# Kernel tuning notes

Hardware: AMD Instinct MI355X
Metric: run time of the kernel (lower is better)

The kernel has to match this reference:

```python
import jax, jax.numpy as jnp
import numpy as np

FEAT_RES = 512
FEAT_DIM = 48
WIDTH = 128
IN_DIM = FEAT_DIM + 27 + 63  # 138
N_RAYS, N_SAMPLES = 4096, 128


def positional_encode(x, L):
    freqs = (2.0 ** jnp.arange(L)).astype(x.dtype)            # [L]
    xf = x[..., None, :] * freqs[:, None]                      # [..., L, 3]
    enc = jnp.concatenate([jnp.sin(xf), jnp.cos(xf)], axis=-1) # [..., L, 6]
    return jnp.concatenate([x, enc.reshape(x.shape[:-1] + (L * 6,))], axis=-1)


def grid_sample_bilinear(plane, gx, gy):
    # plane: [C, H, W]; gx, gy: [N, S] in [-1, 1]; align_corners=True, zeros padding
    H, W = plane.shape[-2], plane.shape[-1]
    ix = (gx + 1.0) * 0.5 * (W - 1)
    iy = (gy + 1.0) * 0.5 * (H - 1)
    x0 = jnp.floor(ix); y0 = jnp.floor(iy)
    x1 = x0 + 1.0;      y1 = y0 + 1.0
    wx1 = ix - x0; wx0 = 1.0 - wx1
    wy1 = iy - y0; wy0 = 1.0 - wy1

    def gather(xi, yi, w):
        valid = (xi >= 0) & (xi <= W - 1) & (yi >= 0) & (yi <= H - 1)
        xc = jnp.clip(xi, 0, W - 1).astype(jnp.int32)
        yc = jnp.clip(yi, 0, H - 1).astype(jnp.int32)
        v = plane[:, yc, xc]                                   # [C, N, S]
        return v * (w * valid.astype(w.dtype))[None]

    return (gather(x0, y0, wx0 * wy0) + gather(x1, y0, wx1 * wy0)
            + gather(x0, y1, wx0 * wy1) + gather(x1, y1, wx1 * wy1))


def setup_inputs() -> dict:
    key = jax.random.key(0)
    ks = jax.random.split(key, 12)
    x = jax.random.uniform(ks[0], (N_RAYS, N_SAMPLES, 3), jnp.float32, -3.0, 3.0)
    d = jax.random.normal(ks[1], (N_RAYS, 3), jnp.float32)
    d = d / jnp.linalg.norm(d, axis=-1, keepdims=True)
    feat = jax.random.normal(ks[2], (3, FEAT_DIM, FEAT_RES, FEAT_RES), jnp.float32)
    s = 0.05
    W0 = jax.random.normal(ks[3], (IN_DIM, WIDTH), jnp.float32) * s
    b0 = jnp.zeros((WIDTH,), jnp.float32)
    W1 = jax.random.normal(ks[4], (WIDTH, WIDTH), jnp.float32) * s
    b1 = jnp.zeros((WIDTH,), jnp.float32)
    W2 = jax.random.normal(ks[5], (WIDTH, WIDTH), jnp.float32) * s
    b2 = jnp.zeros((WIDTH,), jnp.float32)
    W3 = jax.random.normal(ks[6], (WIDTH, 4), jnp.float32) * s
    b3 = jnp.zeros((4,), jnp.float32)
    return {"x": x, "d": d, "feat": feat, "W0": W0, "b0": b0,
            "W1": W1, "b1": b1, "W2": W2, "b2": b2, "W3": W3, "b3": b3}


def reference(x, d, feat, W0, b0, W1, b1, W2, b2, W3, b3):
    x = x / 3.0                                                # [N, S, 3]
    f_xy = grid_sample_bilinear(feat[0], x[..., 0], x[..., 1])  # [C, N, S]
    f_yz = grid_sample_bilinear(feat[1], x[..., 1], x[..., 2])
    f_xz = grid_sample_bilinear(feat[2], x[..., 0], x[..., 2])
    f_sum = jnp.moveaxis(f_xy + f_yz + f_xz, 0, -1)            # [N, S, C]

    d_rep = jnp.broadcast_to(d[:, None, :], x.shape)           # [N, S, 3]
    h = jnp.concatenate([f_sum, positional_encode(d_rep, 4), positional_encode(x, 10)], axis=-1)

    h = jax.nn.relu(h @ W0 + b0)
    h = jax.nn.relu(h @ W1 + b1)
    h = jax.nn.relu(h @ W2 + b2)
    out = h @ W3 + b3                                          # [N, S, 4]
    return jnp.concatenate([out[..., :3], jax.nn.relu(out[..., 3:])], axis=-1)
```

## Files before the change

kernel.cpp:

```cpp
#include <hip/hip_runtime.h>
#include <hip/hip_bf16.h>
#include <hip/hip_fp16.h>
#include <cstdint>
#include <cstddef>

#define NPLANE 262144
#define HSTR 144
#define PW_LAYER 18432
#define NCELL 32768
#define NSAMP 524288
#define NRAY 4096

#define WS_FEAT_OFF 131072
#define FEAT_BYTES  75497472
#define WS_CNT_OFF  (WS_FEAT_OFF + FEAT_BYTES)
#define WS_OFFS_OFF (WS_CNT_OFF + 131072)
#define WS_XS_OFF   (WS_OFFS_OFF + 131072)
#define WS_PED_OFF  (WS_XS_OFF + (size_t)NSAMP*16)
#define WS_END      (WS_PED_OFF + (size_t)NRAY*28*2)

#define TRS_BLKS 3072
#define PREP_BLKS 216
#define PED_BLKS 16
#define K2_BLKS (1 + TRS_BLKS + PREP_BLKS + PED_BLKS)

typedef unsigned int uint;
typedef __attribute__((ext_vector_type(16))) float f32x16;
typedef _Float16 half8 __attribute__((ext_vector_type(8)));

__device__ __forceinline__ unsigned short f16u(float f){
    __half h = __float2half(f);
    return *reinterpret_cast<unsigned short*>(&h);
}
__device__ __forceinline__ f32x16 mfma16_(half8 a, half8 b, f32x16 c){
    return __builtin_amdgcn_mfma_f32_32x32x16_f16(a, b, c, 0,0,0);
}

__device__ __forceinline__ uint part3(uint v){
    v &= 0x3ff;
    v = (v | (v<<16)) & 0x030000FFu;
    v = (v | (v<<8))  & 0x0300F00Fu;
    v = (v | (v<<4))  & 0x030C30C3u;
    v = (v | (v<<2))  & 0x09249249u;
    return v;
}
__device__ __forceinline__ uint cellkey(float x0, float x1, float x2){
    const float s = 1.0f/3.0f;
    const int cx = min(max((int)((x0*s+1.0f)*16.0f),0),31);
    const int cy = min(max((int)((x1*s+1.0f)*16.0f),0),31);
    const int cz = min(max((int)((x2*s+1.0f)*16.0f),0),31);
    return part3((uint)cx) | (part3((uint)cy)<<1) | (part3((uint)cz)<<2);
}

__global__ __launch_bounds__(256) void hist_k(const float* __restrict__ x, uint* __restrict__ counts){
    const int i = blockIdx.x*256 + threadIdx.x;
    if (i >= NSAMP) return;
    atomicAdd(&counts[cellkey(x[3*i], x[3*i+1], x[3*i+2])], 1u);
}

__global__ __launch_bounds__(256) void prepass_k(const float* __restrict__ feat,
                                                 const float* __restrict__ W0,
                                                 const float* __restrict__ W1,
                                                 const float* __restrict__ W2,
                                                 const float* __restrict__ b0,
                                                 const float* __restrict__ b1,
                                                 const float* __restrict__ b2,
                                                 const float* __restrict__ d,
                                                 const uint* __restrict__ counts,
                                                 uint* __restrict__ offs,
                                                 unsigned short* __restrict__ featT,
                                                 unsigned short* __restrict__ wp,
                                                 unsigned short* __restrict__ ped){
    const int bid = blockIdx.x, tid = threadIdx.x;
    if (bid == 0){
        __shared__ uint ps[256];
        uint s = 0;
        for (int i=0;i<128;++i) s += counts[tid*128+i];
        ps[tid] = s; __syncthreads();
        for (int off=1; off<256; off<<=1){
            uint v = (tid>=off) ? ps[tid-off] : 0u;
            __syncthreads();
            ps[tid] += v;
            __syncthreads();
        }
        uint base = ps[tid] - s;
        for (int i=0;i<128;++i){ uint c = counts[tid*128+i]; offs[tid*128+i] = base; base += c; }
        return;
    }
    if (bid <= TRS_BLKS){
        __shared__ unsigned short lb[256*50];
        const int pos = (bid-1)*256 + tid;
        const int p  = pos >> 18;
        const int yx = pos & (NPLANE-1);
        const float* src = feat + (size_t)p*48*NPLANE + yx;
        #pragma unroll 4
        for (int c = 0; c < 48; ++c){
            lb[tid*50 + c] = f16u(src[(size_t)c*NPLANE]);
        }
        __syncthreads();
        uint4* dst = (uint4*)(featT + (size_t)(bid-1)*(256*48));
        #pragma unroll
        for (int m = 0; m < 6; ++m){
            const int u4 = tid + m*256;
            const int byteoff = u4*16;
            const int smp = byteoff/96;
            const int off = (byteoff%96) >> 2;
            const uint* rw = (const uint*)(lb + smp*50);
            uint4 val; val.x = rw[off]; val.y = rw[off+1]; val.z = rw[off+2]; val.w = rw[off+3];
            dst[u4] = val;
        }
        return;
    }
    if (bid <= TRS_BLKS + PREP_BLKS){
        const int idx = (bid - 1 - TRS_BLKS)*256 + tid;
        if (idx >= 3*PW_LAYER) return;
        const int L = idx / PW_LAYER, base = idx % PW_LAYER;
        const float* W = (L==0)? W0 : (L==1)? W1 : W2;
        const float* B = (L==0)? b0 : (L==1)? b1 : b2;
        const int KREAL = (L==0)? 138 : 128;
        const int e  = base & 7;
        const int l  = (base >> 3) & 63;
        const int fr = base >> 9;
        const int ks = fr >> 2, nt = fr & 3;
        const int k  = ks*16 + (l >> 5)*8 + e;
        const int n  = nt*32 + (l & 31);
        float v = 0.f;
        if (k < KREAL) v = W[k*128 + n];
        else if (k == KREAL) v = B[n];
        wp[idx] = f16u(v);
        return;
    }
    {
        const int ray = (bid - 1 - TRS_BLKS - PREP_BLKS)*256 + tid;
        if (ray >= NRAY) return;
        const float dv0 = d[ray*3], dv1 = d[ray*3+1], dv2 = d[ray*3+2];
        unsigned short* row = ped + ray*28;
        row[0]=f16u(dv0); row[1]=f16u(dv1); row[2]=f16u(dv2);
        #pragma unroll
        for (int l=0;l<4;++l){
            const float sc = (float)(1<<l);
            float sv, cv;
            __sincosf(dv0*sc, &sv, &cv); row[3+l*6+0]=f16u(sv); row[3+l*6+3]=f16u(cv);
            __sincosf(dv1*sc, &sv, &cv); row[3+l*6+1]=f16u(sv); row[3+l*6+4]=f16u(cv);
            __sincosf(dv2*sc, &sv, &cv); row[3+l*6+2]=f16u(sv); row[3+l*6+5]=f16u(cv);
        }
        row[27] = 0;
    }
}

__global__ __launch_bounds__(256) void scatter_k(const float* __restrict__ x, uint* __restrict__ offs,
                                                 float4* __restrict__ xs){
    const int i = blockIdx.x*256 + threadIdx.x;
    if (i >= NSAMP) return;
    const float x0 = x[3*i], x1 = x[3*i+1], x2 = x[3*i+2];
    const uint pos = atomicAdd(&offs[cellkey(x0,x1,x2)], 1u);
    xs[pos] = make_float4(x0, x1, x2, __int_as_float(i));
}

__device__ __forceinline__ void run_layer(unsigned short* Hw, const unsigned short* __restrict__ Wp,
                                          int lane, int ln31, int kg, const int* pr){
    const unsigned short* Hrow = Hw + ln31*HSTR;
    f32x16 acc[4];
    #pragma unroll
    for (int i=0;i<4;++i) acc[i] = (f32x16)0.f;
    #pragma unroll
    for (int h=0; h<2; ++h){
        half8 bf[10];
        #pragma unroll
        for (int i=0;i<10;++i){
            const int ks = i>>1, nt = 2*h + (i&1);
            bf[i] = *reinterpret_cast<const half8*>(Wp + (((ks*4+nt)*64 + lane) << 3));
        }
        #pragma unroll
        for (int ks=0; ks<5; ++ks){
            const half8 a = *reinterpret_cast<const half8*>(Hrow + ks*16 + kg*8);
            acc[2*h]   = mfma16_(a, bf[2*ks],   acc[2*h]);
            acc[2*h+1] = mfma16_(a, bf[2*ks+1], acc[2*h+1]);
        }
        #pragma unroll
        for (int i=0;i<8;++i){
            const int ks = 5 + (i>>1), nt = 2*h + (i&1);
            bf[i] = *reinterpret_cast<const half8*>(Wp + (((ks*4+nt)*64 + lane) << 3));
        }
        #pragma unroll
        for (int ks=5; ks<9; ++ks){
            const half8 a = *reinterpret_cast<const half8*>(Hrow + ks*16 + kg*8);
            acc[2*h]   = mfma16_(a, bf[2*(ks-5)],   acc[2*h]);
            acc[2*h+1] = mfma16_(a, bf[2*(ks-5)+1], acc[2*h+1]);
        }
    }
    #pragma unroll
    for (int nt=0;nt<4;++nt){
        #pragma unroll
        for (int r=0;r<16;++r){
            const int row = pr[r] >> 8;
            const int col = nt*32 + (pr[r] & 255);
            Hw[row*HSTR + col] = f16u(fmaxf(acc[nt][r], 0.f));
        }
    }
}

__global__ __launch_bounds__(128, 4) void nerf_mfma(
    const unsigned short* __restrict__ featT,
    const unsigned short* __restrict__ wp0, const unsigned short* __restrict__ wp1,
    const unsigned short* __restrict__ wp2,
    const float* __restrict__ W3, const float* __restrict__ b3,
    const float4* __restrict__ xs, const unsigned short* __restrict__ ped,
    float* __restrict__ out)
{
    __shared__ unsigned short H[64*HSTR];
    __shared__ uint sW3u[256];
    __shared__ float4 sX[64];

    const int tid  = threadIdx.x;
    const int wid  = tid >> 6, lane = tid & 63;
    const int ln31 = lane & 31, kg = lane >> 5;
    const int sbase = wid * 32;
    const int base = (((int)blockIdx.x & 7)*1024 + ((int)blockIdx.x >> 3))*64 + sbase;
    unsigned short* Hw = H + sbase*HSTR;

    half8 pa = (half8)0, pb = (half8)0, qa = (half8)0, qb = (half8)0;
    if (kg == 0){
        pa[0] = (_Float16)(float)ln31;
        pb[0] = (_Float16)1.0f;
        qa[0] = (_Float16)1.0f;
        qb[0] = (_Float16)(float)ln31;
    }
    const f32x16 zz = (f32x16)0.f;
    const f32x16 D1 = mfma16_(pa, pb, zz);
    const f32x16 D2 = mfma16_(qa, qb, zz);
    int pr[16];
    #pragma unroll
    for (int r=0;r<16;++r) pr[r] = (((int)D1[r]) << 8) | (int)D2[r];

    if (lane < 32) sX[sbase + lane] = xs[base + lane];
    #pragma unroll
    for (int j=0;j<2;++j){
        const int idx = lane*2 + j;
        const int i2 = wid*128 + idx;
        const int k = i2 >> 1, c = i2 & 1;
        sW3u[i2] = ((uint)f16u(W3[k*4 + 2*c])) | (((uint)f16u(W3[k*4 + 2*c + 1])) << 16);
    }

    #pragma unroll
    for (int rr=0; rr<2; ++rr){
        if (rr == 1 && lane >= 32) break;
        const int s32 = rr ? lane : ln31;
        const int m   = rr ? 2 : kg;
        const float4 xr = sX[sbase + s32];
        const float xn = ((m==0)? xr.x : (m==1)? xr.y : xr.z) * (1.0f/3.0f);
        unsigned short* row = H + (sbase+s32)*HSTR;
        row[75+m] = f16u(xn);
        float sv, cv;
        __sincosf(xn, &sv, &cv);
        #pragma unroll
        for (int l=0;l<10;++l){
            row[78+l*6+m]   = f16u(sv);
            row[78+l*6+3+m] = f16u(cv);
            const float s2v = 2.0f*sv*cv;
            const float c2v = 1.0f - 2.0f*sv*sv;
            sv = s2v; cv = c2v;
        }
    }

    {
        const int s32 = lane >> 1, hf = lane & 1;
        const int sid = __float_as_int(sX[sbase + s32].w);
        const uint* src = (const uint*)(ped + (sid >> 7)*28) + hf*7;
        uint* dstu = (uint*)(H + (sbase+s32)*HSTR + 48) + hf*7;
        if (hf == 0){
            #pragma unroll
            for (int i=0;i<7;++i) dstu[i] = src[i];
        } else {
            #pragma unroll
            for (int i=0;i<6;++i) dstu[i] = src[i];
            H[(sbase+s32)*HSTR + 74] = ((const unsigned short*)src)[12];
        }
    }

    if (lane < 32){
        *(uint*)(H + (sbase+lane)*HSTR + 138)  = 0x00003C00u;
        *(uint2*)(H + (sbase+lane)*HSTR + 140) = make_uint2(0u, 0u);
    }

    #pragma unroll
    for (int rr=0; rr<3; ++rr){
        const int u = rr*64 + lane;
        const int s32 = u/6, ch = u - s32*6;
        const float4 xr = sX[sbase + s32];
        const float xn0 = xr.x*(1.0f/3.0f);
        const float xn1 = xr.y*(1.0f/3.0f);
        const float xn2 = xr.z*(1.0f/3.0f);
        const int c0 = ch*8;
        __half2 acc[4];
        #pragma unroll
        for (int q=0;q<4;++q) acc[q] = __float2half2_rn(0.f);
        #pragma unroll
        for (int p=0;p<3;++p){
            const float gx = (p==1)? xn1 : xn0;
            const float gy = (p==0)? xn1 : xn2;
            const float ix = ((gx+1.0f)*0.5f)*511.0f;
            const float iy = ((gy+1.0f)*0.5f)*511.0f;
            const float fx0 = floorf(ix), fy0 = floorf(iy);
            const float wx1 = ix - fx0, wy1 = iy - fy0;
            const float wx0 = 1.0f-wx1, wy0 = 1.0f-wy1;
            const int x0i = (int)fx0, y0i = (int)fy0;
            const int x0c = min(max(x0i,0),511),   x1c = min(max(x0i+1,0),511);
            const int y0c = min(max(y0i,0),511),   y1c = min(max(y0i+1,0),511);
            const uint r0 = (uint)(p*NPLANE + y0c*512);
            const uint r1 = (uint)(p*NPLANE + y1c*512);
            const uint  av[4] = {(r0+x0c)*48u, (r0+x1c)*48u, (r1+x0c)*48u, (r1+x1c)*48u};
            const float wv[4] = {wx0*wy0, wx1*wy0, wx0*wy1, wx1*wy1};
            #pragma unroll
            for (int cr=0;cr<4;++cr){
                const uint4 uv = *(const uint4*)(featT + av[cr] + c0);
                const __half2 w2 = __float2half2_rn(wv[cr]);
                union { uint4 v; __half2 h[4]; } t; t.v = uv;
                acc[0] = __hfma2(t.h[0], w2, acc[0]);
                acc[1] = __hfma2(t.h[1], w2, acc[1]);
                acc[2] = __hfma2(t.h[2], w2, acc[2]);
                acc[3] = __hfma2(t.h[3], w2, acc[3]);
            }
        }
        union { __half2 h[4]; uint4 v; } pk;
        #pragma unroll
        for (int q=0;q<4;++q) pk.h[q] = acc[q];
        *(uint4*)(H + (sbase+s32)*HSTR + c0) = pk.v;
    }

    run_layer(Hw, wp0, lane, ln31, kg, pr);
    if (lane < 32) *(uint4*)(Hw + lane*HSTR + 128) = make_uint4(0x00003C00u,0u,0u,0u);
    else           *(uint4*)(Hw + ln31*HSTR + 136) = make_uint4(0u,0u,0u,0u);
    run_layer(Hw, wp1, lane, ln31, kg, pr);
    run_layer(Hw, wp2, lane, ln31, kg, pr);

    {
        const int s32 = lane >> 1, cp = lane & 1;
        const unsigned short* hrow = Hw + s32*HSTR;
        const int sid = __float_as_int(sX[sbase + s32].w);
        const int jp = 2*cp;
        const float2 b3v = *(const float2*)(b3 + jp);
        float a0 = b3v.x, a1 = b3v.y;
        #pragma unroll
        for (int q=0;q<16;++q){
            union { uint4 v; __half2 h[4]; } u;
            u.v = *(const uint4*)(hrow + q*8);
            const int k = q*8;
            #pragma unroll
            for (int j2=0;j2<4;++j2){
                const float2 f = __half22float2(u.h[j2]);
                const int k2 = k + j2*2;
                union { uint u32; __half2 h; } w0c, w1c;
                w0c.u32 = sW3u[(k2+0)*2+cp];
                w1c.u32 = sW3u[(k2+1)*2+cp];
                const float2 w0f = __half22float2(w0c.h);
                const float2 w1f = __half22float2(w1c.h);
                a0 += f.x*w0f.x + f.y*w1f.x;
                a1 += f.x*w0f.y + f.y*w1f.y;
            }
        }
        if (cp == 1) a1 = fmaxf(a1, 0.f);
        float2 o; o.x = a0; o.y = a1;
        *(float2*)(out + (size_t)sid*4 + jp) = o;
    }
}

#define STR 148
#define SBLK 64
template<int K4, int KTAIL>
__device__ __forceinline__ void mlp_layer_fb(float (*Hs)[STR], const float* __restrict__ W,
                                             const float* __restrict__ B, int tid){
    const int tx = tid & 31, ty = tid >> 5;
    const int s0 = ty*8, j0 = tx*4;
    float acc[8][4];
    #pragma unroll
    for (int i=0;i<8;++i){ acc[i][0]=0.f; acc[i][1]=0.f; acc[i][2]=0.f; acc[i][3]=0.f; }
    for (int kk = 0; kk < K4; ++kk){
        const int k = kk*4;
        const float4 wa = *(const float4*)(W + (size_t)(k+0)*128 + j0);
        const float4 wb = *(const float4*)(W + (size_t)(k+1)*128 + j0);
        const float4 wc = *(const float4*)(W + (size_t)(k+2)*128 + j0);
        const float4 wd = *(const float4*)(W + (size_t)(k+3)*128 + j0);
        #pragma unroll
        for (int i=0;i<8;++i){
            const float4 h = *(const float4*)&Hs[s0+i][k];
            acc[i][0] += h.x*wa.x + h.y*wb.x + h.z*wc.x + h.w*wd.x;
            acc[i][1] += h.x*wa.y + h.y*wb.y + h.z*wc.y + h.w*wd.y;
            acc[i][2] += h.x*wa.z + h.y*wb.z + h.z*wc.z + h.w*wd.z;
            acc[i][3] += h.x*wa.w + h.y*wb.w + h.z*wc.w + h.w*wd.w;
        }
    }
    #pragma unroll
    for (int t=0;t<KTAIL;++t){
        const int k = K4*4+t;
        const float4 wa = *(const float4*)(W + (size_t)k*128 + j0);
        #pragma unroll
        for (int i=0;i<8;++i){
            const float h = Hs[s0+i][k];
            acc[i][0] += h*wa.x; acc[i][1] += h*wa.y; acc[i][2] += h*wa.z; acc[i][3] += h*wa.w;
        }
    }
    const float4 bb = *(const float4*)(B + j0);
    __syncthreads();
    #pragma unroll
    for (int i=0;i<8;++i){
        float4 o;
        o.x = fmaxf(acc[i][0]+bb.x, 0.f);
        o.y = fmaxf(acc[i][1]+bb.y, 0.f);
        o.z = fmaxf(acc[i][2]+bb.z, 0.f);
        o.w = fmaxf(acc[i][3]+bb.w, 0.f);
        *(float4*)&Hs[s0+i][j0] = o;
    }
    __syncthreads();
}

__global__ __launch_bounds__(256) void nerf_fused_fb(
    const float* __restrict__ x, const float* __restrict__ d,
    const float* __restrict__ feat,
    const float* __restrict__ W0, const float* __restrict__ b0,
    const float* __restrict__ W1, const float* __restrict__ b1,
    const float* __restrict__ W2, const float* __restrict__ b2,
    const float* __restrict__ W3, const float* __restrict__ b3,
    float* __restrict__ out)
{
    __shared__ float Hs[SBLK][STR];
    __shared__ uint4  sA[3][SBLK];
    __shared__ float4 sW[3][SBLK];

    const int tid = threadIdx.x;
    const int g0 = blockIdx.x * SBLK;

    if (tid < 192){
        const int s = tid & 63, p = tid >> 6;
        const int g = g0 + s;
        const float xn0 = x[3*g+0]/3.0f, xn1 = x[3*g+1]/3.0f, xn2 = x[3*g+2]/3.0f;
        const float gx = (p==1)? xn1 : xn0;
        const float gy = (p==0)? xn1 : xn2;
        const float ix = ((gx+1.0f)*0.5f)*511.0f;
        const float iy = ((gy+1.0f)*0.5f)*511.0f;
        const float fx0 = floorf(ix), fy0 = floorf(iy);
        const float wx1 = ix - fx0, wy1 = iy - fy0;
        const float wx0 = 1.0f-wx1, wy0 = 1.0f-wy1;
        const int x0i = (int)fx0, y0i = (int)fy0;
        const int x0c = min(max(x0i,0),511),   x1c = min(max(x0i+1,0),511);
        const int y0c = min(max(y0i,0),511),   y1c = min(max(y0i+1,0),511);
        const uint bp = (uint)p*48u*NPLANE;
        sA[p][s] = make_uint4(bp + y0c*512 + x0c, bp + y0c*512 + x1c,
                              bp + y1c*512 + x0c, bp + y1c*512 + x1c);
        sW[p][s] = make_float4(wx0*wy0, wx1*wy0, wx0*wy1, wx1*wy1);
    }
    if (tid < 64){
        const int s = tid, g = g0 + s;
        float xn[3];
        xn[0]=x[3*g+0]/3.0f; xn[1]=x[3*g+1]/3.0f; xn[2]=x[3*g+2]/3.0f;
        Hs[s][75]=xn[0]; Hs[s][76]=xn[1]; Hs[s][77]=xn[2];
        float f = 1.0f;
        for (int l=0;l<10;++l){
            #pragma unroll
            for (int m=0;m<3;++m){
                const float a = xn[m]*f;
                Hs[s][78+l*6+m]   = sinf(a);
                Hs[s][78+l*6+3+m] = cosf(a);
            }
            f *= 2.0f;
        }
    } else if (tid < 91){
        const int k = tid-64;
        const int ray = g0 >> 7;
        float v;
        if (k < 3) v = d[ray*3+k];
        else {
            const int l=(k-3)/6, r=(k-3)%6;
            const float a = d[ray*3 + (r%3)] * (float)(1<<l);
            v = (r<3)? sinf(a) : cosf(a);
        }
        for (int s2=0;s2<64;++s2) Hs[s2][48+k]=v;
    }
    __syncthreads();

    for (int it = tid; it < 384; it += 256){
        const int s = it & 63;
        const int c0 = (it >> 6)*8;
        float acc[8];
        #pragma unroll
        for (int q=0;q<8;++q) acc[q]=0.f;
        #pragma unroll
        for (int p=0;p<3;++p){
            const uint4  aa = sA[p][s];
            const float4 ww = sW[p][s];
            const uint  av[4] = {aa.x,aa.y,aa.z,aa.w};
            const float wv[4] = {ww.x,ww.y,ww.z,ww.w};
            #pragma unroll
            for (int cr=0;cr<4;++cr){
                const float w = wv[cr];
                const float* bsrc = feat + av[cr] + (size_t)c0*NPLANE;
                #pragma unroll
                for (int q=0;q<8;++q) acc[q] += w*bsrc[(size_t)q*NPLANE];
            }
        }
        *(float4*)&Hs[s][c0]   = make_float4(acc[0],acc[1],acc[2],acc[3]);
        *(float4*)&Hs[s][c0+4] = make_float4(acc[4],acc[5],acc[6],acc[7]);
    }
    __syncthreads();

    mlp_layer_fb<34,2>(Hs, W0, b0, tid);
    mlp_layer_fb<32,0>(Hs, W1, b1, tid);
    mlp_layer_fb<32,0>(Hs, W2, b2, tid);

    {
        const int s = tid>>2, j = tid&3;
        float acc = 0.f;
        for (int kk=0; kk<32; ++kk){
            const float4 h = *(const float4*)&Hs[s][kk*4];
            const int k = kk*4;
            acc += h.x*W3[(k+0)*4+j] + h.y*W3[(k+1)*4+j]
                 + h.z*W3[(k+2)*4+j] + h.w*W3[(k+3)*4+j];
        }
        acc += b3[j];
        if (j==3) acc = fmaxf(acc, 0.f);
        out[(size_t)blockIdx.x*256 + tid] = acc;
    }
}

extern "C" void kernel_launch(void* const* d_in, const int* in_sizes, int n_in,
                              void* d_out, int out_size, void* d_ws, size_t ws_size,
                              hipStream_t stream){
    (void)in_sizes; (void)n_in; (void)out_size;
    const float* x    = (const float*)d_in[0];
    const float* ddir = (const float*)d_in[1];
    const float* feat = (const float*)d_in[2];
    const float* W0 = (const float*)d_in[3];  const float* b0 = (const float*)d_in[4];
    const float* W1 = (const float*)d_in[5];  const float* b1 = (const float*)d_in[6];
    const float* W2 = (const float*)d_in[7];  const float* b2 = (const float*)d_in[8];
    const float* W3 = (const float*)d_in[9];  const float* b3 = (const float*)d_in[10];
    float* out = (float*)d_out;

    char* wsb = (char*)d_ws;

    if (ws_size >= WS_END){
        unsigned short* wsu   = (unsigned short*)wsb;
        unsigned short* featT = (unsigned short*)(wsb + WS_FEAT_OFF);
        uint*   counts = (uint*)(wsb + WS_CNT_OFF);
        uint*   offs   = (uint*)(wsb + WS_OFFS_OFF);
        float4* xsrec  = (float4*)(wsb + WS_XS_OFF);
        unsigned short* ped = (unsigned short*)(wsb + WS_PED_OFF);
        hipMemsetAsync(counts, 0, NCELL*sizeof(uint), stream);
        hist_k<<<2048, 256, 0, stream>>>(x, counts);
        prepass_k<<<K2_BLKS, 256, 0, stream>>>(feat, W0, W1, W2, b0, b1, b2, ddir,
                                               counts, offs, featT, wsu, ped);
        scatter_k<<<2048, 256, 0, stream>>>(x, offs, xsrec);
        nerf_mfma<<<8192, 128, 0, stream>>>(featT,
                                            wsu, wsu + PW_LAYER, wsu + 2*PW_LAYER,
                                            W3, b3, xsrec, ped, out);
    } else {
        nerf_fused_fb<<<8192, 256, 0, stream>>>(x, ddir, feat,
                                                W0,b0,W1,b1,W2,b2,W3,b3, out);
    }
}
```

Before: 272.0 us.

## Split prefix scan out, fold scatter into prepass, halve MFMA accumulator live set

Moves the cell-count prefix scan into its own single-block kernel so the scatter work can be merged into the prepass launch, running scatter blocks alongside the feature transpose and weight packing. In the MLP layers, each half of the output columns now gets its own accumulator pair, and the first half's results are packed into half2 registers before the second pass. This lowers peak accumulator register pressure and could raise occupancy. The per-block W3 staging into shared memory is removed and the final layer reads fp32 W3 directly from global memory, which adds global loads in the epilogue.

```diff
diff --git a/kernel.cpp b/kernel.cpp
--- a/kernel.cpp
+++ b/kernel.cpp
@@ -22,7 +22,8 @@
 #define TRS_BLKS 3072
 #define PREP_BLKS 216
 #define PED_BLKS 16
-#define K2_BLKS (1 + TRS_BLKS + PREP_BLKS + PED_BLKS)
+#define SCAT_BLKS 2048
+#define K2_BLKS (TRS_BLKS + PREP_BLKS + PED_BLKS + SCAT_BLKS)
 
 typedef unsigned int uint;
 typedef __attribute__((ext_vector_type(16))) float f32x16;
@@ -56,6 +57,22 @@
     const int i = blockIdx.x*256 + threadIdx.x;
     if (i >= NSAMP) return;
     atomicAdd(&counts[cellkey(x[3*i], x[3*i+1], x[3*i+2])], 1u);
+}
+
+__global__ __launch_bounds__(256) void scan_k(const uint* __restrict__ counts, uint* __restrict__ offs){
+    __shared__ uint ps[256];
+    const int tid = threadIdx.x;
+    uint s = 0;
+    for (int i=0;i<128;++i) s += counts[tid*128+i];
+    ps[tid] = s; __syncthreads();
+    for (int off=1; off<256; off<<=1){
+        uint v = (tid>=off) ? ps[tid-off] : 0u;
+        __syncthreads();
+        ps[tid] += v;
+        __syncthreads();
+    }
+    uint base = ps[tid] - s;
+    for (int i=0;i<128;++i){ uint c = counts[tid*128+i]; offs[tid*128+i] = base; base += c; }
 }
 
 __global__ __launch_bounds__(256) void prepass_k(const float* __restrict__ feat,
@@ -66,30 +83,16 @@
                                                  const float* __restrict__ b1,
                                                  const float* __restrict__ b2,
                                                  const float* __restrict__ d,
-                                                 const uint* __restrict__ counts,
+                                                 const float* __restrict__ x,
                                                  uint* __restrict__ offs,
                                                  unsigned short* __restrict__ featT,
                                                  unsigned short* __restrict__ wp,
-                                                 unsigned short* __restrict__ ped){
+                                                 unsigned short* __restrict__ ped,
+                                                 float4* __restrict__ xs){
     const int bid = blockIdx.x, tid = threadIdx.x;
-    if (bid == 0){
-        __shared__ uint ps[256];
-        uint s = 0;
-        for (int i=0;i<128;++i) s += counts[tid*128+i];
-        ps[tid] = s; __syncthreads();
-        for (int off=1; off<256; off<<=1){
-            uint v = (tid>=off) ? ps[tid-off] : 0u;
-            __syncthreads();
-            ps[tid] += v;
-            __syncthreads();
-        }
-        uint base = ps[tid] - s;
-        for (int i=0;i<128;++i){ uint c = counts[tid*128+i]; offs[tid*128+i] = base; base += c; }
-        return;
-    }
-    if (bid <= TRS_BLKS){
+    if (bid < TRS_BLKS){
         __shared__ unsigned short lb[256*50];
-        const int pos = (bid-1)*256 + tid;
+        const int pos = bid*256 + tid;
         const int p  = pos >> 18;
         const int yx = pos & (NPLANE-1);
         const float* src = feat + (size_t)p*48*NPLANE + yx;
@@ -98,7 +101,7 @@
             lb[tid*50 + c] = f16u(src[(size_t)c*NPLANE]);
         }
         __syncthreads();
-        uint4* dst = (uint4*)(featT + (size_t)(bid-1)*(256*48));
+        uint4* dst = (uint4*)(featT + (size_t)bid*(256*48));
         #pragma unroll
         for (int m = 0; m < 6; ++m){
             const int u4 = tid + m*256;
@@ -111,8 +114,8 @@
         }
         return;
     }
-    if (bid <= TRS_BLKS + PREP_BLKS){
-        const int idx = (bid - 1 - TRS_BLKS)*256 + tid;
+    if (bid < TRS_BLKS + PREP_BLKS){
+        const int idx = (bid - TRS_BLKS)*256 + tid;
         if (idx >= 3*PW_LAYER) return;
         const int L = idx / PW_LAYER, base = idx % PW_LAYER;
         const float* W = (L==0)? W0 : (L==1)? W1 : W2;
@@ -130,8 +133,8 @@
         wp[idx] = f16u(v);
         return;
     }
-    {
-        const int ray = (bid - 1 - TRS_BLKS - PREP_BLKS)*256 + tid;
+    if (bid < TRS_BLKS + PREP_BLKS + PED_BLKS){
+        const int ray = (bid - TRS_BLKS - PREP_BLKS)*256 + tid;
         if (ray >= NRAY) return;
         const float dv0 = d[ray*3], dv1 = d[ray*3+1], dv2 = d[ray*3+2];
         unsigned short* row = ped + ray*28;
@@ -145,58 +148,68 @@
             __sincosf(dv2*sc, &sv, &cv); row[3+l*6+2]=f16u(sv); row[3+l*6+5]=f16u(cv);
         }
         row[27] = 0;
-    }
-}
-
-__global__ __launch_bounds__(256) void scatter_k(const float* __restrict__ x, uint* __restrict__ offs,
-                                                 float4* __restrict__ xs){
-    const int i = blockIdx.x*256 + threadIdx.x;
-    if (i >= NSAMP) return;
-    const float x0 = x[3*i], x1 = x[3*i+1], x2 = x[3*i+2];
-    const uint pos = atomicAdd(&offs[cellkey(x0,x1,x2)], 1u);
-    xs[pos] = make_float4(x0, x1, x2, __int_as_float(i));
+        return;
+    }
+    {
+        const int i = (bid - TRS_BLKS - PREP_BLKS - PED_BLKS)*256 + tid;
+        if (i >= NSAMP) return;
+        const float x0 = x[3*i], x1 = x[3*i+1], x2 = x[3*i+2];
+        const uint pos = atomicAdd(&offs[cellkey(x0,x1,x2)], 1u);
+        xs[pos] = make_float4(x0, x1, x2, __int_as_float(i));
+    }
+}
+
+__device__ __forceinline__ void half_pass(const unsigned short* Hrow,
+                                          const unsigned short* __restrict__ Wp,
+                                          int h, int lane, int kg, f32x16 acc[2]){
+    acc[0] = (f32x16)0.f; acc[1] = (f32x16)0.f;
+    half8 bf[10];
+    #pragma unroll
+    for (int i=0;i<10;++i){
+        const int ks = i>>1, nt = 2*h + (i&1);
+        bf[i] = *reinterpret_cast<const half8*>(Wp + (((ks*4+nt)*64 + lane) << 3));
+    }
+    #pragma unroll
+    for (int ks=0; ks<5; ++ks){
+        const half8 a = *reinterpret_cast<const half8*>(Hrow + ks*16 + kg*8);
+        acc[0] = mfma16_(a, bf[2*ks],   acc[0]);
+        acc[1] = mfma16_(a, bf[2*ks+1], acc[1]);
+    }
+    #pragma unroll
+    for (int i=0;i<8;++i){
+        const int ks = 5 + (i>>1), nt = 2*h + (i&1);
+        bf[i] = *reinterpret_cast<const half8*>(Wp + (((ks*4+nt)*64 + lane) << 3));
+    }
+    #pragma unroll
+    for (int ks=5; ks<9; ++ks){
+        const half8 a = *reinterpret_cast<const half8*>(Hrow + ks*16 + kg*8);
+        acc[0] = mfma16_(a, bf[2*(ks-5)],   acc[0]);
+        acc[1] = mfma16_(a, bf[2*(ks-5)+1], acc[1]);
+    }
 }
 
 __device__ __forceinline__ void run_layer(unsigned short* Hw, const unsigned short* __restrict__ Wp,
                                           int lane, int ln31, int kg, const int* pr){
     const unsigned short* Hrow = Hw + ln31*HSTR;
-    f32x16 acc[4];
-    #pragma unroll
-    for (int i=0;i<4;++i) acc[i] = (f32x16)0.f;
-    #pragma unroll
-    for (int h=0; h<2; ++h){
-        half8 bf[10];
-        #pragma unroll
-        for (int i=0;i<10;++i){
-            const int ks = i>>1, nt = 2*h + (i&1);
-            bf[i] = *reinterpret_cast<const half8*>(Wp + (((ks*4+nt)*64 + lane) << 3));
-        }
-        #pragma unroll
-        for (int ks=0; ks<5; ++ks){
-            const half8 a = *reinterpret_cast<const half8*>(Hrow + ks*16 + kg*8);
-            acc[2*h]   = mfma16_(a, bf[2*ks],   acc[2*h]);
-            acc[2*h+1] = mfma16_(a, bf[2*ks+1], acc[2*h+1]);
-        }
-        #pragma unroll
-        for (int i=0;i<8;++i){
-            const int ks = 5 + (i>>1), nt = 2*h + (i&1);
-            bf[i] = *reinterpret_cast<const half8*>(Wp + (((ks*4+nt)*64 + lane) << 3));
-        }
-        #pragma unroll
-        for (int ks=5; ks<9; ++ks){
-            const half8 a = *reinterpret_cast<const half8*>(Hrow + ks*16 + kg*8);
-            acc[2*h]   = mfma16_(a, bf[2*(ks-5)],   acc[2*h]);
-            acc[2*h+1] = mfma16_(a, bf[2*(ks-5)+1], acc[2*h+1]);
-        }
-    }
-    #pragma unroll
-    for (int nt=0;nt<4;++nt){
-        #pragma unroll
-        for (int r=0;r<16;++r){
-            const int row = pr[r] >> 8;
-            const int col = nt*32 + (pr[r] & 255);
-            Hw[row*HSTR + col] = f16u(fmaxf(acc[nt][r], 0.f));
-        }
+    f32x16 acc[2];
+    half_pass(Hrow, Wp, 0, lane, kg, acc);
+    uint p0[16];
+    #pragma unroll
+    for (int r=0;r<16;++r){
+        const __half2 hv = __floats2half2_rn(fmaxf(acc[0][r],0.f), fmaxf(acc[1][r],0.f));
+        p0[r] = *reinterpret_cast<const uint*>(&hv);
+    }
+    half_pass(Hrow, Wp, 1, lane, kg, acc);
+    #pragma unroll
+    for (int r=0;r<16;++r){
+        const int row = pr[r] >> 8;
+        const int col = pr[r] & 255;
+        unsigned short* hr = Hw + row*HSTR + col;
+        const uint v0 = p0[r];
+        hr[0]   = (unsigned short)(v0 & 0xffffu);
+        hr[32]  = (unsigned short)(v0 >> 16);
+        hr[64]  = f16u(fmaxf(acc[0][r], 0.f));
+        hr[96]  = f16u(fmaxf(acc[1][r], 0.f));
     }
 }
 
@@ -209,7 +222,6 @@
     float* __restrict__ out)
 {
     __shared__ unsigned short H[64*HSTR];
-    __shared__ uint sW3u[256];
     __shared__ float4 sX[64];
 
     const int tid  = threadIdx.x;
@@ -234,13 +246,6 @@
     for (int r=0;r<16;++r) pr[r] = (((int)D1[r]) << 8) | (int)D2[r];
 
     if (lane < 32) sX[sbase + lane] = xs[base + lane];
-    #pragma unroll
-    for (int j=0;j<2;++j){
-        const int idx = lane*2 + j;
-        const int i2 = wid*128 + idx;
-        const int k = i2 >> 1, c = i2 & 1;
-        sW3u[i2] = ((uint)f16u(W3[k*4 + 2*c])) | (((uint)f16u(W3[k*4 + 2*c + 1])) << 16);
-    }
 
     #pragma unroll
     for (int rr=0; rr<2; ++rr){
@@ -350,11 +355,8 @@
             for (int j2=0;j2<4;++j2){
                 const float2 f = __half22float2(u.h[j2]);
                 const int k2 = k + j2*2;
-                union { uint u32; __half2 h; } w0c, w1c;
-                w0c.u32 = sW3u[(k2+0)*2+cp];
-                w1c.u32 = sW3u[(k2+1)*2+cp];
-                const float2 w0f = __half22float2(w0c.h);
-                const float2 w1f = __half22float2(w1c.h);
+                const float2 w0f = *(const float2*)(W3 + (k2+0)*4 + jp);
+                const float2 w1f = *(const float2*)(W3 + (k2+1)*4 + jp);
                 a0 += f.x*w0f.x + f.y*w1f.x;
                 a1 += f.x*w0f.y + f.y*w1f.y;
             }
@@ -546,9 +548,9 @@
         unsigned short* ped = (unsigned short*)(wsb + WS_PED_OFF);
         hipMemsetAsync(counts, 0, NCELL*sizeof(uint), stream);
         hist_k<<<2048, 256, 0, stream>>>(x, counts);
-        prepass_k<<<K2_BLKS, 256, 0, stream>>>(feat, W0, W1, W2, b0, b1, b2, ddir,
-                                               counts, offs, featT, wsu, ped);
-        scatter_k<<<2048, 256, 0, stream>>>(x, offs, xsrec);
+        scan_k<<<1, 256, 0, stream>>>(counts, offs);
+        prepass_k<<<K2_BLKS, 256, 0, stream>>>(feat, W0, W1, W2, b0, b1, b2, ddir, x,
+                                               offs, featT, wsu, ped, xsrec);
         nerf_mfma<<<8192, 128, 0, stream>>>(featT,
                                             wsu, wsu + PW_LAYER, wsu + 2*PW_LAYER,
                                             W3, b3, xsrec, ped, out);
```

New measurement: 304.3 us. 1.12x slower.
